# Kernel optimization log

Hardware: AMD Instinct MI355X
Metric: run time of the kernel (lower is better)

Reference implementation:

```python
import jax, jax.numpy as jnp
import numpy as np

EOS_ID = 2
PAD_ID = 0


def setup_inputs() -> dict:
    key = jax.random.key(0)
    ks = jax.random.split(key, 10)
    B, E, H, V, T = 64, 512, 512, 32000, 20
    features = jax.random.normal(ks[0], (B, E), dtype=jnp.float32)
    captions = jax.random.randint(ks[1], (B, T), 0, V)            # unused in policy branch
    lengths = jax.random.randint(ks[2], (B,), 1, T + 1)
    lengths = lengths.at[0].set(T)                                 # make max(lengths) == 20 deterministic
    # parameters (match torch init scales roughly)
    embed_W = jax.random.uniform(ks[3], (V, E), jnp.float32, -0.1, 0.1)
    s = 1.0 / np.sqrt(H)
    W_ih = jax.random.uniform(ks[4], (4 * H, E), jnp.float32, -s, s)
    W_hh = jax.random.uniform(ks[5], (4 * H, H), jnp.float32, -s, s)
    b_ih = jax.random.uniform(ks[6], (4 * H,), jnp.float32, -s, s)
    b_hh = jax.random.uniform(ks[7], (4 * H,), jnp.float32, -s, s)
    linear_W = jax.random.uniform(ks[8], (V, H), jnp.float32, -0.1, 0.1)
    linear_b = jnp.zeros((V,), jnp.float32)
    return {"features": features, "captions": captions, "lengths": lengths,
            "use_policy": 1, "embed_W": embed_W, "W_ih": W_ih, "W_hh": W_hh,
            "b_ih": b_ih, "b_hh": b_hh, "linear_W": linear_W, "linear_b": linear_b}


def _lstm_cell(x, h, c, W_ih, W_hh, b_ih, b_hh):
    # PyTorch gate order: i, f, g, o
    gates = x @ W_ih.T + b_ih + h @ W_hh.T + b_hh        # [B, 4H]
    i, f, g, o = jnp.split(gates, 4, axis=-1)
    i, f, o = jax.nn.sigmoid(i), jax.nn.sigmoid(f), jax.nn.sigmoid(o)
    g = jnp.tanh(g)
    c = f * c + i * g
    h = o * jnp.tanh(c)
    return h, c


def reference(features, captions, lengths, use_policy, embed_W, W_ih, W_hh,
              b_ih, b_hh, linear_W, linear_b):
    # LSTM decode with categorical sampling, stopping per-example at EOS (id 2)
    # and padding remaining steps with id 0 / log_prob 0. The original loops
    # over batch and time with batch-size-1 kernels; here we batch + lax.scan.
    B, H = features.shape[0], W_hh.shape[1]
    T = int(jnp.max(lengths))                            # concrete at trace setup
    step_keys = jax.random.split(jax.random.key(42), T)

    def step(carry, key_t):
        h, c, x, done = carry
        h, c = _lstm_cell(x, h, c, W_ih, W_hh, b_ih, b_hh)
        logits = h @ linear_W.T + linear_b               # [B, V]
        logp = jax.nn.log_softmax(logits, axis=-1)
        tok = jax.random.categorical(key_t, logits)      # [B] int32
        lp = jnp.take_along_axis(logp, tok[:, None], axis=1)[:, 0]
        ids_rec = jnp.where(done, PAD_ID, tok)
        lp_rec = jnp.where(done, 0.0, lp)
        done = done | ((tok == EOS_ID) & ~done)          # EOS token itself is recorded
        x = embed_W[tok]                                 # next-step input embedding
        return (h, c, x, done), (ids_rec, lp_rec)

    init = (jnp.zeros((B, H), features.dtype), jnp.zeros((B, H), features.dtype),
            features, jnp.zeros((B,), bool))
    _, (ids, logps) = jax.lax.scan(step, init, step_keys)
    sampled_ids = jnp.transpose(ids)                     # [B, T]
    saved_log_probs = jnp.transpose(logps)               # [B, T]
    return sampled_ids, saved_log_probs
```

## Files before the change

kernel.cpp:

```cpp
#include <hip/hip_runtime.h>
#include <hip/hip_bf16.h>
#include <stdint.h>
#include <float.h>

#define BB 64
#define EE 512
#define HH 512
#define VV 32000
#define TT 20
#define INV2048 0.00048828125f

typedef _Float16 f16x8 __attribute__((ext_vector_type(8)));
typedef float f32x4 __attribute__((ext_vector_type(4)));

__device__ __host__ __forceinline__ void tf2x32(uint32_t k0, uint32_t k1, uint32_t x0, uint32_t x1,
                                                uint32_t& o0, uint32_t& o1) {
  const uint32_t k2 = k0 ^ k1 ^ 0x1BD11BDAu;
  x0 += k0; x1 += k1;
#define RND(R) { x0 += x1; x1 = (x1 << R) | (x1 >> (32 - R)); x1 ^= x0; }
  RND(13) RND(15) RND(26) RND(6)
  x0 += k1; x1 += k2 + 1u;
  RND(17) RND(29) RND(16) RND(24)
  x0 += k2; x1 += k0 + 2u;
  RND(13) RND(15) RND(26) RND(6)
  x0 += k0; x1 += k1 + 3u;
  RND(17) RND(29) RND(16) RND(24)
  x0 += k1; x1 += k2 + 4u;
  RND(13) RND(15) RND(26) RND(6)
  x0 += k2; x1 += k0 + 5u;
#undef RND
  o0 = x0; o1 = x1;
}

__device__ __forceinline__ float gumbel_for(uint32_t k1t, uint32_t k2t, uint32_t idx) {
  uint32_t o0, o1; tf2x32(k1t, k2t, 0u, idx, o0, o1);
  uint32_t bits = o0 ^ o1;
  uint32_t mant = bits >> 9;
  float f = __uint_as_float(0x3f800000u | mant) - 1.0f;
  float u = mant ? f : 1.1754943508222875e-38f;
  return -logf(-logf(u));
}

struct Part { float bv; int bix; float blog; float m; float s; };

__device__ __forceinline__ void part_combine(Part& P, const Part& Q) {
  if (Q.bv > P.bv || (Q.bv == P.bv && Q.bix < P.bix)) { P.bv = Q.bv; P.bix = Q.bix; P.blog = Q.blog; }
  if (Q.m > P.m) { P.s = P.s * expf(P.m - Q.m) + Q.s; P.m = Q.m; }
  else           { P.s += Q.s * expf(Q.m - P.m); }
}

__global__ __launch_bounds__(256) void k_init(float* __restrict__ hA, float* __restrict__ cT,
                                              int* __restrict__ done) {
  int i = blockIdx.x * 256 + threadIdx.x;
  if (i < HH * BB) { hA[i] = 0.f; cT[i] = 0.f; }
  if (i < BB) done[i] = 0;
}

__global__ __launch_bounds__(256) void k_gates(const float* __restrict__ xin,
                                               const float* __restrict__ hT,
                                               const float* __restrict__ Wih,
                                               const float* __restrict__ Whh,
                                               float* __restrict__ gatesP) {
  const int jt = blockIdx.x;
  const int kc = blockIdx.y;
  const int tx = threadIdx.x;
  __shared__ float a[64][64];
  __shared__ float wj[64][68];
  const int bi = (tx & 15) * 4;
  const int ji = (tx >> 4) * 4;
  float acc[4][4] = {};
  const float* Wsrc = (kc < 4) ? Wih : Whh;
  for (int s = 0; s < 2; ++s) {
    const int kg = kc * 128 + s * 64;
    if (kc < 4) {
      #pragma unroll
      for (int r = 0; r < 4; ++r) {
        int fi = r * 256 + tx;
        int b = fi >> 4, k4 = (fi & 15) * 4;
        const float4 v = *(const float4*)(xin + b * EE + kg + k4);
        a[k4 + 0][b] = v.x; a[k4 + 1][b] = v.y; a[k4 + 2][b] = v.z; a[k4 + 3][b] = v.w;
      }
    } else {
      #pragma unroll
      for (int r = 0; r < 4; ++r) {
        int fi = r * 256 + tx;
        int row = fi >> 4, c4 = (fi & 15) * 4;
        *(float4*)(&a[row][c4]) = *(const float4*)(hT + (kg - 512 + row) * BB + c4);
      }
    }
    const int kcol = kg & 511;
    #pragma unroll
    for (int r = 0; r < 4; ++r) {
      int fi = r * 256 + tx;
      int j = fi >> 4, k4 = (fi & 15) * 4;
      const float4 v = *(const float4*)(Wsrc + (size_t)(jt * 64 + j) * EE + kcol + k4);
      wj[k4 + 0][j] = v.x; wj[k4 + 1][j] = v.y; wj[k4 + 2][j] = v.z; wj[k4 + 3][j] = v.w;
    }
    __syncthreads();
    #pragma unroll 8
    for (int kk = 0; kk < 64; ++kk) {
      const float4 av = *(const float4*)(&a[kk][bi]);
      const float4 wv = *(const float4*)(&wj[kk][ji]);
      const float avx[4] = {av.x, av.y, av.z, av.w};
      const float wvx[4] = {wv.x, wv.y, wv.z, wv.w};
      #pragma unroll
      for (int jj = 0; jj < 4; ++jj)
        #pragma unroll
        for (int bb = 0; bb < 4; ++bb)
          acc[jj][bb] = fmaf(wvx[jj], avx[bb], acc[jj][bb]);
    }
    __syncthreads();
  }
  #pragma unroll
  for (int jj = 0; jj < 4; ++jj) {
    float4 o = make_float4(acc[jj][0], acc[jj][1], acc[jj][2], acc[jj][3]);
    *(float4*)(gatesP + ((size_t)kc * 2048 + jt * 64 + ji + jj) * BB + bi) = o;
  }
}

__global__ __launch_bounds__(256) void k_lstm_update(const float* __restrict__ gatesP,
                                                     const float* __restrict__ b_ih,
                                                     const float* __restrict__ b_hh,
                                                     float* __restrict__ cT,
                                                     float* __restrict__ hT) {
  const int blk = blockIdx.x;
  const int tx = threadIdx.x;
  const int b = tx & 63;
  const int dk = tx >> 6;
  #pragma unroll
  for (int r = 0; r < 2; ++r) {
    const int k = blk * 8 + dk + r * 4;
    float g[4];
    #pragma unroll
    for (int gi = 0; gi < 4; ++gi) {
      const int j = gi * 512 + k;
      float s = 0.f;
      #pragma unroll
      for (int kc = 0; kc < 8; ++kc) s += gatesP[((size_t)kc * 2048 + j) * BB + b];
      g[gi] = s + b_ih[j] + b_hh[j];
    }
    const float ig = 1.f / (1.f + expf(-g[0]));
    const float fg = 1.f / (1.f + expf(-g[1]));
    const float gg = tanhf(g[2]);
    const float og = 1.f / (1.f + expf(-g[3]));
    const float c = fg * cT[k * BB + b] + ig * gg;
    cT[k * BB + b] = c;
    hT[k * BB + b] = og * tanhf(c);
  }
}

__global__ __launch_bounds__(256) void k_lstm_update_frag(const float* __restrict__ gatesP,
                                                          const float* __restrict__ b_ih,
                                                          const float* __restrict__ b_hh,
                                                          float* __restrict__ cT,
                                                          float* __restrict__ hT,
                                                          _Float16* __restrict__ hfh,
                                                          _Float16* __restrict__ hfl) {
  const int blk = blockIdx.x;
  const int tx = threadIdx.x;
  const int b = tx & 63;
  const int dk = tx >> 6;
  #pragma unroll
  for (int r = 0; r < 2; ++r) {
    const int k = blk * 8 + dk + r * 4;
    float g[4];
    #pragma unroll
    for (int gi = 0; gi < 4; ++gi) {
      const int j = gi * 512 + k;
      float s = 0.f;
      #pragma unroll
      for (int kc = 0; kc < 8; ++kc) s += gatesP[((size_t)kc * 2048 + j) * BB + b];
      g[gi] = s + b_ih[j] + b_hh[j];
    }
    const float ig = 1.f / (1.f + expf(-g[0]));
    const float fg = 1.f / (1.f + expf(-g[1]));
    const float gg = tanhf(g[2]);
    const float og = 1.f / (1.f + expf(-g[3]));
    const float c = fg * cT[k * BB + b] + ig * gg;
    cT[k * BB + b] = c;
    const float h = og * tanhf(c);
    hT[k * BB + b] = h;
    const _Float16 hh = (_Float16)h;
    const _Float16 hl = (_Float16)((h - (float)hh) * 2048.0f);
    const int cc = k >> 5, kr = k & 31;
    const int lane = (kr >> 3) * 16 + (b & 15), j = kr & 7, nb = b >> 4;
    const int idx = ((cc * 4 + nb) * 64 + lane) * 8 + j;
    hfh[idx] = hh; hfl[idx] = hl;
  }
}

__global__ __launch_bounds__(256) void k_convW2(const float* __restrict__ LW,
                                                _Float16* __restrict__ Wh,
                                                _Float16* __restrict__ Wl) {
  const int bv = blockIdx.x, bk = blockIdx.y;
  const int tx = threadIdx.x;
  __shared__ float lds[64][65];
  #pragma unroll
  for (int r = 0; r < 4; ++r) {
    const int fi = r * 256 + tx;
    const int vl = fi >> 4, k4 = (fi & 15) * 4;
    const float4 v = *(const float4*)(LW + (size_t)(bv * 64 + vl) * HH + bk * 64 + k4);
    lds[vl][k4] = v.x; lds[vl][k4 + 1] = v.y; lds[vl][k4 + 2] = v.z; lds[vl][k4 + 3] = v.w;
  }
  __syncthreads();
  #pragma unroll
  for (int r = 0; r < 2; ++r) {
    const int u = r * 256 + tx;
    const int frag = u >> 6;
    const int vbl = frag >> 1, cl = frag & 1;
    const int lane = u & 63;
    const int m = lane & 15, lh = lane >> 4;
    f16x8 hi, lo;
    #pragma unroll
    for (int j = 0; j < 8; ++j) {
      const float f = lds[vbl * 16 + m][cl * 32 + lh * 8 + j];
      const _Float16 h = (_Float16)f;
      hi[j] = h;
      lo[j] = (_Float16)((f - (float)h) * 2048.0f);
    }
    const size_t o = (((size_t)(bv * 4 + vbl) * 16 + (bk * 2 + cl)) * 64 + lane) * 8;
    *(f16x8*)(Wh + o) = hi;
    *(f16x8*)(Wl + o) = lo;
  }
}

__global__ __launch_bounds__(256) void k_logits4(const f16x8* __restrict__ Wh,
                                                 const f16x8* __restrict__ Wl,
                                                 const f16x8* __restrict__ hfh,
                                                 const f16x8* __restrict__ hfl,
                                                 const float* __restrict__ lb,
                                                 uint32_t k1t, uint32_t k2t,
                                                 float4* __restrict__ pf4,
                                                 int* __restrict__ pidx) {
  const int wv = threadIdx.x >> 6;
  const int vt = blockIdx.x * 4 + wv;
  const int lane = threadIdx.x & 63;
  __shared__ float red[4][64][5];
  const f32x4 zero = {0.f, 0.f, 0.f, 0.f};
  f32x4 aH[4]  = {zero, zero, zero, zero};
  f32x4 aM1[4] = {zero, zero, zero, zero};
  f32x4 aM2[4] = {zero, zero, zero, zero};
  const size_t wbase = (size_t)vt * 16 * 64 + lane;
  f16x8 whC = Wh[wbase], wlC = Wl[wbase];
  #pragma unroll 4
  for (int c = 0; c < 16; ++c) {
    f16x8 whN, wlN;
    if (c < 15) { whN = Wh[wbase + (c + 1) * 64]; wlN = Wl[wbase + (c + 1) * 64]; }
    #pragma unroll
    for (int nb = 0; nb < 4; ++nb) {
      const f16x8 bh = hfh[(c * 4 + nb) * 64 + lane];
      const f16x8 bl = hfl[(c * 4 + nb) * 64 + lane];
      aH[nb]  = __builtin_amdgcn_mfma_f32_16x16x32_f16(whC, bh, aH[nb], 0, 0, 0);
      aM1[nb] = __builtin_amdgcn_mfma_f32_16x16x32_f16(whC, bl, aM1[nb], 0, 0, 0);
      aM2[nb] = __builtin_amdgcn_mfma_f32_16x16x32_f16(wlC, bh, aM2[nb], 0, 0, 0);
    }
    whC = whN; wlC = wlN;
  }
  const int v0 = vt * 16 + ((lane >> 4) << 2);
  const float4 bias = *(const float4*)(lb + v0);
  const float bb4[4] = {bias.x, bias.y, bias.z, bias.w};
  Part P[4];
  #pragma unroll
  for (int nb = 0; nb < 4; ++nb) {
    const int b = nb * 16 + (lane & 15);
    float lg = aH[nb][0] + (aM1[nb][0] + aM2[nb][0]) * INV2048 + bb4[0];
    Part p;
    p.bv = lg + gumbel_for(k1t, k2t, (uint32_t)(b * VV + v0));
    p.bix = v0; p.blog = lg; p.m = lg; p.s = 1.0f;
    #pragma unroll
    for (int reg = 1; reg < 4; ++reg) {
      float lg2 = aH[nb][reg] + (aM1[nb][reg] + aM2[nb][reg]) * INV2048 + bb4[reg];
      float pe = lg2 + gumbel_for(k1t, k2t, (uint32_t)(b * VV + v0 + reg));
      if (pe > p.bv) { p.bv = pe; p.bix = v0 + reg; p.blog = lg2; }
      if (lg2 > p.m) { p.s = p.s * expf(p.m - lg2) + 1.f; p.m = lg2; }
      else           { p.s += expf(lg2 - p.m); }
    }
    P[nb] = p;
  }
  #pragma unroll
  for (int msk = 16; msk <= 32; msk <<= 1) {
    #pragma unroll
    for (int nb = 0; nb < 4; ++nb) {
      Part Q;
      Q.bv   = __shfl_xor(P[nb].bv, msk, 64);
      Q.bix  = __shfl_xor(P[nb].bix, msk, 64);
      Q.blog = __shfl_xor(P[nb].blog, msk, 64);
      Q.m    = __shfl_xor(P[nb].m, msk, 64);
      Q.s    = __shfl_xor(P[nb].s, msk, 64);
      part_combine(P[nb], Q);
    }
  }
  if (lane < 16) {
    #pragma unroll
    for (int nb = 0; nb < 4; ++nb) {
      const int b = nb * 16 + lane;
      red[wv][b][0] = P[nb].bv; red[wv][b][1] = __int_as_float(P[nb].bix);
      red[wv][b][2] = P[nb].blog; red[wv][b][3] = P[nb].m; red[wv][b][4] = P[nb].s;
    }
  }
  __syncthreads();
  if (threadIdx.x < 64) {
    const int b = threadIdx.x;
    Part Pc;
    Pc.bv = red[0][b][0]; Pc.bix = __float_as_int(red[0][b][1]); Pc.blog = red[0][b][2];
    Pc.m = red[0][b][3]; Pc.s = red[0][b][4];
    #pragma unroll
    for (int w = 1; w < 4; ++w) {
      Part Q;
      Q.bv = red[w][b][0]; Q.bix = __float_as_int(red[w][b][1]); Q.blog = red[w][b][2];
      Q.m = red[w][b][3]; Q.s = red[w][b][4];
      part_combine(Pc, Q);
    }
    pf4[(size_t)blockIdx.x * BB + b] = make_float4(Pc.bv, Pc.blog, Pc.m, Pc.s);
    pidx[blockIdx.x * BB + b] = Pc.bix;
  }
}

__global__ __launch_bounds__(128) void k_logits2(const float* __restrict__ hT,
                                                 const float* __restrict__ LW,
                                                 const float* __restrict__ lb,
                                                 uint32_t k1t, uint32_t k2t,
                                                 float4* __restrict__ pf4,
                                                 int* __restrict__ pidx) {
  const int vt = blockIdx.x;
  const int tx = threadIdx.x;
  __shared__ float lds[5120];
  float* wTs = lds;
  const int vthr = tx & 15;
  const int bthr = tx >> 4;
  const int vi = vthr * 2;
  const int bi = bthr * 8;
  const int vq = tx >> 4;
  const int ks = tx & 15;
  float acc[2][8] = {};
  for (int kt = 0; kt < 8; ++kt) {
    const int kg = kt * 64;
    #pragma unroll
    for (int s = 0; s < 4; ++s) {
      const int kk = ks + 16 * s;
      const size_t rb = (size_t)(vt * 32 + 4 * vq) * HH + kg + kk;
      float w0 = LW[rb];
      float w1 = LW[rb + HH];
      float w2 = LW[rb + 2 * HH];
      float w3 = LW[rb + 3 * HH];
      const int ph = (4 * vq) ^ (4 * (kk & 7));
      *(float4*)&wTs[kk * 32 + ph] = make_float4(w0, w1, w2, w3);
    }
    __syncthreads();
    #pragma unroll 4
    for (int kk = 0; kk < 64; ++kk) {
      const float* hrow = hT + (size_t)(kg + kk) * BB;
      const float4 h0 = *(const float4*)(hrow + bi);
      const float4 h1 = *(const float4*)(hrow + bi + 4);
      const float2 wv = *(const float2*)&wTs[kk * 32 + (vi ^ (4 * (kk & 7)))];
      acc[0][0] = fmaf(wv.x, h0.x, acc[0][0]); acc[0][1] = fmaf(wv.x, h0.y, acc[0][1]);
      acc[0][2] = fmaf(wv.x, h0.z, acc[0][2]); acc[0][3] = fmaf(wv.x, h0.w, acc[0][3]);
      acc[0][4] = fmaf(wv.x, h1.x, acc[0][4]); acc[0][5] = fmaf(wv.x, h1.y, acc[0][5]);
      acc[0][6] = fmaf(wv.x, h1.z, acc[0][6]); acc[0][7] = fmaf(wv.x, h1.w, acc[0][7]);
      acc[1][0] = fmaf(wv.y, h0.x, acc[1][0]); acc[1][1] = fmaf(wv.y, h0.y, acc[1][1]);
      acc[1][2] = fmaf(wv.y, h0.z, acc[1][2]); acc[1][3] = fmaf(wv.y, h0.w, acc[1][3]);
      acc[1][4] = fmaf(wv.y, h1.x, acc[1][4]); acc[1][5] = fmaf(wv.y, h1.y, acc[1][5]);
      acc[1][6] = fmaf(wv.y, h1.z, acc[1][6]); acc[1][7] = fmaf(wv.y, h1.w, acc[1][7]);
    }
    __syncthreads();
  }
  const int v0g = vt * 32 + vi;
  const float bias0 = lb[v0g];
  const float bias1 = lb[v0g + 1];
  float* red = lds;
  #pragma unroll
  for (int bb = 0; bb < 8; ++bb) {
    const int b = bi + bb;
    const float lg0 = acc[0][bb] + bias0;
    const float lg1 = acc[1][bb] + bias1;
    Part p;
    p.bv = lg0 + gumbel_for(k1t, k2t, (uint32_t)(b * VV + v0g));
    p.bix = v0g; p.blog = lg0;
    const float pe1 = lg1 + gumbel_for(k1t, k2t, (uint32_t)(b * VV + v0g + 1));
    if (pe1 > p.bv) { p.bv = pe1; p.bix = v0g + 1; p.blog = lg1; }
    if (lg0 >= lg1) { p.m = lg0; p.s = 1.f + expf(lg1 - lg0); }
    else            { p.m = lg1; p.s = 1.f + expf(lg0 - lg1); }
    const int slot = (b * 16 + vthr) * 5;
    red[slot + 0] = p.bv; red[slot + 1] = __int_as_float(p.bix); red[slot + 2] = p.blog;
    red[slot + 3] = p.m;  red[slot + 4] = p.s;
  }
  __syncthreads();
  if (tx < 64) {
    const int b = tx;
    Part P;
    { const int s0 = (b * 16) * 5;
      P.bv = red[s0]; P.bix = __float_as_int(red[s0 + 1]); P.blog = red[s0 + 2];
      P.m = red[s0 + 3]; P.s = red[s0 + 4]; }
    #pragma unroll
    for (int c = 1; c < 16; ++c) {
      const int s0 = (b * 16 + c) * 5;
      Part Q; Q.bv = red[s0]; Q.bix = __float_as_int(red[s0 + 1]); Q.blog = red[s0 + 2];
      Q.m = red[s0 + 3]; Q.s = red[s0 + 4];
      part_combine(P, Q);
    }
    pf4[(size_t)vt * BB + b] = make_float4(P.bv, P.blog, P.m, P.s);
    pidx[vt * BB + b] = P.bix;
  }
}

__global__ __launch_bounds__(256) void k_sample2(const float4* __restrict__ pf4,
                                                 const int* __restrict__ pidx,
                                                 const float* __restrict__ embW,
                                                 int* __restrict__ done,
                                                 float* __restrict__ x,
                                                 float* __restrict__ out,
                                                 int step, int nvt) {
  const int b = blockIdx.x;
  const int tx = threadIdx.x;
  __shared__ float red[256 * 5];
  __shared__ int stok;
  Part p; p.bv = -FLT_MAX; p.bix = 0x7fffffff; p.blog = 0.f; p.m = -FLT_MAX; p.s = 0.f;
  for (int vt = tx; vt < nvt; vt += 256) {
    float4 q = pf4[(size_t)vt * BB + b];
    Part Q; Q.bv = q.x; Q.blog = q.y; Q.m = q.z; Q.s = q.w; Q.bix = pidx[vt * BB + b];
    part_combine(p, Q);
  }
  red[tx * 5 + 0] = p.bv; red[tx * 5 + 1] = __int_as_float(p.bix); red[tx * 5 + 2] = p.blog;
  red[tx * 5 + 3] = p.m;  red[tx * 5 + 4] = p.s;
  __syncthreads();
  for (int st = 128; st > 0; st >>= 1) {
    if (tx < st) {
      const int s0 = tx * 5, s1 = (tx + st) * 5;
      Part P, Q;
      P.bv = red[s0]; P.bix = __float_as_int(red[s0 + 1]); P.blog = red[s0 + 2]; P.m = red[s0 + 3]; P.s = red[s0 + 4];
      Q.bv = red[s1]; Q.bix = __float_as_int(red[s1 + 1]); Q.blog = red[s1 + 2]; Q.m = red[s1 + 3]; Q.s = red[s1 + 4];
      part_combine(P, Q);
      red[s0] = P.bv; red[s0 + 1] = __int_as_float(P.bix); red[s0 + 2] = P.blog; red[s0 + 3] = P.m; red[s0 + 4] = P.s;
    }
    __syncthreads();
  }
  if (tx == 0) {
    const int tok = __float_as_int(red[1]);
    const float blog = red[2], M = red[3], S = red[4];
    const float lp = blog - (M + logf(S));
    const int dn = done[b];
    out[b * TT + step] = dn ? 0.0f : (float)tok;
    out[BB * TT + b * TT + step] = dn ? 0.0f : lp;
    done[b] = dn | (tok == 2);
    stok = tok;
  }
  __syncthreads();
  const int tok = stok;
  for (int e = tx; e < EE; e += 256) x[b * EE + e] = embW[(size_t)tok * EE + e];
}

extern "C" void kernel_launch(void* const* d_in, const int* in_sizes, int n_in,
                              void* d_out, int out_size, void* d_ws, size_t ws_size,
                              hipStream_t stream) {
  const float* features = (const float*)d_in[0];
  const float* embW     = (const float*)d_in[4];
  const float* Wih      = (const float*)d_in[5];
  const float* Whh      = (const float*)d_in[6];
  const float* bih      = (const float*)d_in[7];
  const float* bhh      = (const float*)d_in[8];
  const float* LW       = (const float*)d_in[9];
  const float* lb       = (const float*)d_in[10];
  float* out = (float*)d_out;

  uint32_t keys[TT][2];
  for (int t = 0; t < TT; ++t) tf2x32(0u, 42u, 0u, (uint32_t)t, keys[t][0], keys[t][1]);

  float* ws = (float*)d_ws;
  float* hA = ws;
  float* hB = ws + 32768;
  float* cT = ws + 65536;
  float* x  = ws + 98304;

  if (ws_size >= (size_t)73000000) {
    float*  gatesP = ws + 131072;
    float4* pf4    = (float4*)(ws + 1179648);
    int*    pidx   = (int*)(ws + 1691648);
    int*    done   = (int*)(ws + 1819648);
    _Float16* hfh  = (_Float16*)(ws + 1819712);
    _Float16* hfl  = (_Float16*)(ws + 1836096);
    _Float16* Whi  = (_Float16*)(ws + 1852480);
    _Float16* Wlo  = (_Float16*)(ws + 10044480);

    k_convW2<<<dim3(500, 8), dim3(256), 0, stream>>>(LW, Whi, Wlo);
    k_init<<<dim3(128), dim3(256), 0, stream>>>(hA, cT, done);
    const float* hin = hA;
    float* hout = hB;
    for (int t = 0; t < TT; ++t) {
      const float* xin = (t == 0) ? features : x;
      k_gates<<<dim3(32, 8), dim3(256), 0, stream>>>(xin, hin, Wih, Whh, gatesP);
      k_lstm_update_frag<<<dim3(64), dim3(256), 0, stream>>>(gatesP, bih, bhh, cT, hout, hfh, hfl);
      k_logits4<<<dim3(500), dim3(256), 0, stream>>>((const f16x8*)Whi, (const f16x8*)Wlo,
                                                     (const f16x8*)hfh, (const f16x8*)hfl,
                                                     lb, keys[t][0], keys[t][1], pf4, pidx);
      k_sample2<<<dim3(64), dim3(256), 0, stream>>>(pf4, pidx, embW, done, x, out, t, 500);
      const float* tmp = hout; hout = (float*)hin; hin = tmp;
    }
  } else {
    float*  gatesP = ws + 131072;
    float4* pf4    = (float4*)(ws + 131072 + 1048576);
    int*    pidx   = (int*)(ws + 131072 + 1048576 + 256000);
    int*    done   = (int*)(ws + 131072 + 1048576 + 256000 + 64000);

    k_init<<<dim3(128), dim3(256), 0, stream>>>(hA, cT, done);
    const float* hin = hA;
    float* hout = hB;
    for (int t = 0; t < TT; ++t) {
      const float* xin = (t == 0) ? features : x;
      k_gates<<<dim3(32, 8), dim3(256), 0, stream>>>(xin, hin, Wih, Whh, gatesP);
      k_lstm_update<<<dim3(64), dim3(256), 0, stream>>>(gatesP, bih, bhh, cT, hout);
      k_logits2<<<dim3(1000), dim3(128), 0, stream>>>(hout, LW, lb, keys[t][0], keys[t][1], pf4, pidx);
      k_sample2<<<dim3(64), dim3(256), 0, stream>>>(pf4, pidx, embW, done, x, out, t, 1000);
      const float* tmp = hout; hout = (float*)hin; hin = tmp;
    }
  }
}
```

Measured before the change: 935.3 us.

## Fuse LSTM gate GEMM and cell update into split-fp16 MFMA kernel

Replaces the FP32 SIMT gates GEMM plus separate reduction/update kernel with one MFMA kernel. It uses split hi/lo fp16 weights, converted once up front, and a concatenated [x;h] operand held in MFMA fragment layout. The sampler now writes the next-step embedding straight into that fragment layout, and the cell kernel writes h into it, which removes the gatesP partial-sum round trip and one launch per step. The risks are the cell kernel's low occupancy (only 32 blocks) and a precision change from the 3-product split-fp16 scheme. The workspace threshold is raised, so this path only runs when the workspace is at least 80 MB.

```diff
diff --git a/kernel.cpp b/kernel.cpp
--- a/kernel.cpp
+++ b/kernel.cpp
@@ -48,6 +48,326 @@
   if (Q.m > P.m) { P.s = P.s * expf(P.m - Q.m) + Q.s; P.m = Q.m; }
   else           { P.s += Q.s * expf(Q.m - P.m); }
 }
+
+
+__global__ __launch_bounds__(256) void k_convW2(const float* __restrict__ LW,
+                                                _Float16* __restrict__ Wh,
+                                                _Float16* __restrict__ Wl) {
+  const int bv = blockIdx.x, bk = blockIdx.y;
+  const int tx = threadIdx.x;
+  __shared__ float lds[64][65];
+  #pragma unroll
+  for (int r = 0; r < 4; ++r) {
+    const int fi = r * 256 + tx;
+    const int vl = fi >> 4, k4 = (fi & 15) * 4;
+    const float4 v = *(const float4*)(LW + (size_t)(bv * 64 + vl) * HH + bk * 64 + k4);
+    lds[vl][k4] = v.x; lds[vl][k4 + 1] = v.y; lds[vl][k4 + 2] = v.z; lds[vl][k4 + 3] = v.w;
+  }
+  __syncthreads();
+  #pragma unroll
+  for (int r = 0; r < 2; ++r) {
+    const int u = r * 256 + tx;
+    const int frag = u >> 6;
+    const int vbl = frag >> 1, cl = frag & 1;
+    const int lane = u & 63;
+    const int m = lane & 15, lh = lane >> 4;
+    f16x8 hi, lo;
+    #pragma unroll
+    for (int j = 0; j < 8; ++j) {
+      const float f = lds[vbl * 16 + m][cl * 32 + lh * 8 + j];
+      const _Float16 h = (_Float16)f;
+      hi[j] = h;
+      lo[j] = (_Float16)((f - (float)h) * 2048.0f);
+    }
+    const size_t o = (((size_t)(bv * 4 + vbl) * 16 + (bk * 2 + cl)) * 64 + lane) * 8;
+    *(f16x8*)(Wh + o) = hi;
+    *(f16x8*)(Wl + o) = lo;
+  }
+}
+
+__global__ __launch_bounds__(256) void k_convG(const float* __restrict__ Wih,
+                                               const float* __restrict__ Whh,
+                                               _Float16* __restrict__ Gh,
+                                               _Float16* __restrict__ Gl) {
+  const int bv = blockIdx.x, bk = blockIdx.y;
+  const int tx = threadIdx.x;
+  __shared__ float lds[64][65];
+  const float* src = (bk < 8) ? Wih : Whh;
+  const int col = (bk < 8) ? bk * 64 : (bk - 8) * 64;
+  #pragma unroll
+  for (int r = 0; r < 4; ++r) {
+    const int fi = r * 256 + tx;
+    const int jl = fi >> 4, k4 = (fi & 15) * 4;
+    const float4 v = *(const float4*)(src + (size_t)(bv * 64 + jl) * 512 + col + k4);
+    lds[jl][k4] = v.x; lds[jl][k4 + 1] = v.y; lds[jl][k4 + 2] = v.z; lds[jl][k4 + 3] = v.w;
+  }
+  __syncthreads();
+  #pragma unroll
+  for (int r = 0; r < 2; ++r) {
+    const int u = r * 256 + tx;
+    const int frag = u >> 6;
+    const int vbl = frag >> 1, cl = frag & 1;
+    const int lane = u & 63;
+    const int m = lane & 15, lh = lane >> 4;
+    f16x8 hi, lo;
+    #pragma unroll
+    for (int j = 0; j < 8; ++j) {
+      const float f = lds[vbl * 16 + m][cl * 32 + lh * 8 + j];
+      const _Float16 h = (_Float16)f;
+      hi[j] = h;
+      lo[j] = (_Float16)((f - (float)h) * 2048.0f);
+    }
+    const size_t o = (((size_t)(bv * 4 + vbl) * 32 + (bk * 2 + cl)) * 64 + lane) * 8;
+    *(f16x8*)(Gh + o) = hi;
+    *(f16x8*)(Gl + o) = lo;
+  }
+}
+
+__global__ __launch_bounds__(256) void k_convX(const float* __restrict__ feat,
+                                               _Float16* __restrict__ xh,
+                                               _Float16* __restrict__ xl) {
+  const int t = blockIdx.x * 256 + threadIdx.x;
+  const int b = t >> 9, e = t & 511;
+  const float f = feat[t];
+  const _Float16 hh = (_Float16)f;
+  const _Float16 hl = (_Float16)((f - (float)hh) * 2048.0f);
+  const int cc = e >> 5, lane2 = ((e & 31) >> 3) * 16 + (b & 15), j2 = e & 7, nb2 = b >> 4;
+  const int fidx = ((cc * 4 + nb2) * 64 + lane2) * 8 + j2;
+  xh[fidx] = hh; xl[fidx] = hl;
+}
+
+__global__ __launch_bounds__(256) void k_init2(float* __restrict__ cT,
+                                               float* __restrict__ xh0f,
+                                               float* __restrict__ xl0f,
+                                               int* __restrict__ done) {
+  const int i = blockIdx.x * 256 + threadIdx.x;
+  cT[i] = 0.f;
+  if (i < 16384) { xh0f[16384 + i] = 0.f; xl0f[16384 + i] = 0.f; }
+  if (i < BB) done[i] = 0;
+}
+
+__global__ __launch_bounds__(256) void k_cell_mfma(const f16x8* __restrict__ Gh,
+                                                   const f16x8* __restrict__ Gl,
+                                                   const f16x8* __restrict__ xbh,
+                                                   const f16x8* __restrict__ xbl,
+                                                   const float* __restrict__ bih,
+                                                   const float* __restrict__ bhh,
+                                                   float* __restrict__ cT,
+                                                   _Float16* __restrict__ hfh,
+                                                   _Float16* __restrict__ hfl,
+                                                   _Float16* __restrict__ nxh,
+                                                   _Float16* __restrict__ nxl) {
+  const int kt = blockIdx.x;
+  const int g = threadIdx.x >> 6;
+  const int lane = threadIdx.x & 63;
+  const int vb = g * 32 + kt;
+  __shared__ float gl[4][16][64];
+  const f32x4 zero = {0.f, 0.f, 0.f, 0.f};
+  f32x4 aH[4]  = {zero, zero, zero, zero};
+  f32x4 aM1[4] = {zero, zero, zero, zero};
+  f32x4 aM2[4] = {zero, zero, zero, zero};
+  const size_t wbase = (size_t)vb * 32 * 64 + lane;
+  f16x8 whC = Gh[wbase], wlC = Gl[wbase];
+  #pragma unroll 4
+  for (int c = 0; c < 32; ++c) {
+    f16x8 whN, wlN;
+    if (c < 31) { whN = Gh[wbase + (c + 1) * 64]; wlN = Gl[wbase + (c + 1) * 64]; }
+    #pragma unroll
+    for (int nb = 0; nb < 4; ++nb) {
+      const f16x8 bh = xbh[(c * 4 + nb) * 64 + lane];
+      const f16x8 bl = xbl[(c * 4 + nb) * 64 + lane];
+      aH[nb]  = __builtin_amdgcn_mfma_f32_16x16x32_f16(whC, bh, aH[nb], 0, 0, 0);
+      aM1[nb] = __builtin_amdgcn_mfma_f32_16x16x32_f16(whC, bl, aM1[nb], 0, 0, 0);
+      aM2[nb] = __builtin_amdgcn_mfma_f32_16x16x32_f16(wlC, bh, aM2[nb], 0, 0, 0);
+    }
+    whC = whN; wlC = wlN;
+  }
+  const int jl0 = (lane >> 4) << 2;
+  const int j0 = g * 512 + kt * 16 + jl0;
+  const float4 bi4 = *(const float4*)(bih + j0);
+  const float4 bh4 = *(const float4*)(bhh + j0);
+  const float bsum[4] = {bi4.x + bh4.x, bi4.y + bh4.y, bi4.z + bh4.z, bi4.w + bh4.w};
+  #pragma unroll
+  for (int nb = 0; nb < 4; ++nb) {
+    const int bcol = nb * 16 + (lane & 15);
+    #pragma unroll
+    for (int reg = 0; reg < 4; ++reg) {
+      gl[g][jl0 + reg][bcol] = aH[nb][reg] + (aM1[nb][reg] + aM2[nb][reg]) * INV2048 + bsum[reg];
+    }
+  }
+  __syncthreads();
+  #pragma unroll
+  for (int r = 0; r < 4; ++r) {
+    const int idx = r * 256 + threadIdx.x;
+    const int kloc = idx >> 6, b = idx & 63;
+    const float gi = gl[0][kloc][b];
+    const float gf = gl[1][kloc][b];
+    const float gg = gl[2][kloc][b];
+    const float go = gl[3][kloc][b];
+    const float ig = 1.f / (1.f + expf(-gi));
+    const float fg = 1.f / (1.f + expf(-gf));
+    const float gv = tanhf(gg);
+    const float og = 1.f / (1.f + expf(-go));
+    const int k = kt * 16 + kloc;
+    const float c = fg * cT[k * BB + b] + ig * gv;
+    cT[k * BB + b] = c;
+    const float h = og * tanhf(c);
+    const _Float16 hh = (_Float16)h;
+    const _Float16 hl = (_Float16)((h - (float)hh) * 2048.0f);
+    const int cc = k >> 5, lane2 = ((k & 31) >> 3) * 16 + (b & 15), j2 = k & 7, nb2 = b >> 4;
+    const int fidx = ((cc * 4 + nb2) * 64 + lane2) * 8 + j2;
+    hfh[fidx] = hh; hfl[fidx] = hl;
+    const int fidx2 = (((16 + cc) * 4 + nb2) * 64 + lane2) * 8 + j2;
+    nxh[fidx2] = hh; nxl[fidx2] = hl;
+  }
+}
+
+__global__ __launch_bounds__(256) void k_logits4(const f16x8* __restrict__ Wh,
+                                                 const f16x8* __restrict__ Wl,
+                                                 const f16x8* __restrict__ hfh,
+                                                 const f16x8* __restrict__ hfl,
+                                                 const float* __restrict__ lb,
+                                                 uint32_t k1t, uint32_t k2t,
+                                                 float4* __restrict__ pf4,
+                                                 int* __restrict__ pidx) {
+  const int wv = threadIdx.x >> 6;
+  const int vt = blockIdx.x * 4 + wv;
+  const int lane = threadIdx.x & 63;
+  __shared__ float red[4][64][5];
+  const f32x4 zero = {0.f, 0.f, 0.f, 0.f};
+  f32x4 aH[4]  = {zero, zero, zero, zero};
+  f32x4 aM1[4] = {zero, zero, zero, zero};
+  f32x4 aM2[4] = {zero, zero, zero, zero};
+  const size_t wbase = (size_t)vt * 16 * 64 + lane;
+  f16x8 whC = Wh[wbase], wlC = Wl[wbase];
+  #pragma unroll 4
+  for (int c = 0; c < 16; ++c) {
+    f16x8 whN, wlN;
+    if (c < 15) { whN = Wh[wbase + (c + 1) * 64]; wlN = Wl[wbase + (c + 1) * 64]; }
+    #pragma unroll
+    for (int nb = 0; nb < 4; ++nb) {
+      const f16x8 bh = hfh[(c * 4 + nb) * 64 + lane];
+      const f16x8 bl = hfl[(c * 4 + nb) * 64 + lane];
+      aH[nb]  = __builtin_amdgcn_mfma_f32_16x16x32_f16(whC, bh, aH[nb], 0, 0, 0);
+      aM1[nb] = __builtin_amdgcn_mfma_f32_16x16x32_f16(whC, bl, aM1[nb], 0, 0, 0);
+      aM2[nb] = __builtin_amdgcn_mfma_f32_16x16x32_f16(wlC, bh, aM2[nb], 0, 0, 0);
+    }
+    whC = whN; wlC = wlN;
+  }
+  const int v0 = vt * 16 + ((lane >> 4) << 2);
+  const float4 bias = *(const float4*)(lb + v0);
+  const float bb4[4] = {bias.x, bias.y, bias.z, bias.w};
+  Part P[4];
+  #pragma unroll
+  for (int nb = 0; nb < 4; ++nb) {
+    const int b = nb * 16 + (lane & 15);
+    float lg = aH[nb][0] + (aM1[nb][0] + aM2[nb][0]) * INV2048 + bb4[0];
+    Part p;
+    p.bv = lg + gumbel_for(k1t, k2t, (uint32_t)(b * VV + v0));
+    p.bix = v0; p.blog = lg; p.m = lg; p.s = 1.0f;
+    #pragma unroll
+    for (int reg = 1; reg < 4; ++reg) {
+      float lg2 = aH[nb][reg] + (aM1[nb][reg] + aM2[nb][reg]) * INV2048 + bb4[reg];
+      float pe = lg2 + gumbel_for(k1t, k2t, (uint32_t)(b * VV + v0 + reg));
+      if (pe > p.bv) { p.bv = pe; p.bix = v0 + reg; p.blog = lg2; }
+      if (lg2 > p.m) { p.s = p.s * expf(p.m - lg2) + 1.f; p.m = lg2; }
+      else           { p.s += expf(lg2 - p.m); }
+    }
+    P[nb] = p;
+  }
+  #pragma unroll
+  for (int msk = 16; msk <= 32; msk <<= 1) {
+    #pragma unroll
+    for (int nb = 0; nb < 4; ++nb) {
+      Part Q;
+      Q.bv   = __shfl_xor(P[nb].bv, msk, 64);
+      Q.bix  = __shfl_xor(P[nb].bix, msk, 64);
+      Q.blog = __shfl_xor(P[nb].blog, msk, 64);
+      Q.m    = __shfl_xor(P[nb].m, msk, 64);
+      Q.s    = __shfl_xor(P[nb].s, msk, 64);
+      part_combine(P[nb], Q);
+    }
+  }
+  if (lane < 16) {
+    #pragma unroll
+    for (int nb = 0; nb < 4; ++nb) {
+      const int b = nb * 16 + lane;
+      red[wv][b][0] = P[nb].bv; red[wv][b][1] = __int_as_float(P[nb].bix);
+      red[wv][b][2] = P[nb].blog; red[wv][b][3] = P[nb].m; red[wv][b][4] = P[nb].s;
+    }
+  }
+  __syncthreads();
+  if (threadIdx.x < 64) {
+    const int b = threadIdx.x;
+    Part Pc;
+    Pc.bv = red[0][b][0]; Pc.bix = __float_as_int(red[0][b][1]); Pc.blog = red[0][b][2];
+    Pc.m = red[0][b][3]; Pc.s = red[0][b][4];
+    #pragma unroll
+    for (int w = 1; w < 4; ++w) {
+      Part Q;
+      Q.bv = red[w][b][0]; Q.bix = __float_as_int(red[w][b][1]); Q.blog = red[w][b][2];
+      Q.m = red[w][b][3]; Q.s = red[w][b][4];
+      part_combine(Pc, Q);
+    }
+    pf4[(size_t)blockIdx.x * BB + b] = make_float4(Pc.bv, Pc.blog, Pc.m, Pc.s);
+    pidx[blockIdx.x * BB + b] = Pc.bix;
+  }
+}
+
+__global__ __launch_bounds__(256) void k_sample3(const float4* __restrict__ pf4,
+                                                 const int* __restrict__ pidx,
+                                                 const float* __restrict__ embW,
+                                                 int* __restrict__ done,
+                                                 _Float16* __restrict__ nxh,
+                                                 _Float16* __restrict__ nxl,
+                                                 float* __restrict__ out,
+                                                 int step) {
+  const int b = blockIdx.x;
+  const int tx = threadIdx.x;
+  __shared__ float red[256 * 5];
+  __shared__ int stok;
+  Part p; p.bv = -FLT_MAX; p.bix = 0x7fffffff; p.blog = 0.f; p.m = -FLT_MAX; p.s = 0.f;
+  for (int vt = tx; vt < 500; vt += 256) {
+    float4 q = pf4[(size_t)vt * BB + b];
+    Part Q; Q.bv = q.x; Q.blog = q.y; Q.m = q.z; Q.s = q.w; Q.bix = pidx[vt * BB + b];
+    part_combine(p, Q);
+  }
+  red[tx * 5 + 0] = p.bv; red[tx * 5 + 1] = __int_as_float(p.bix); red[tx * 5 + 2] = p.blog;
+  red[tx * 5 + 3] = p.m;  red[tx * 5 + 4] = p.s;
+  __syncthreads();
+  for (int st = 128; st > 0; st >>= 1) {
+    if (tx < st) {
+      const int s0 = tx * 5, s1 = (tx + st) * 5;
+      Part P, Q;
+      P.bv = red[s0]; P.bix = __float_as_int(red[s0 + 1]); P.blog = red[s0 + 2]; P.m = red[s0 + 3]; P.s = red[s0 + 4];
+      Q.bv = red[s1]; Q.bix = __float_as_int(red[s1 + 1]); Q.blog = red[s1 + 2]; Q.m = red[s1 + 3]; Q.s = red[s1 + 4];
+      part_combine(P, Q);
+      red[s0] = P.bv; red[s0 + 1] = __int_as_float(P.bix); red[s0 + 2] = P.blog; red[s0 + 3] = P.m; red[s0 + 4] = P.s;
+    }
+    __syncthreads();
+  }
+  if (tx == 0) {
+    const int tok = __float_as_int(red[1]);
+    const float blog = red[2], M = red[3], S = red[4];
+    const float lp = blog - (M + logf(S));
+    const int dn = done[b];
+    out[b * TT + step] = dn ? 0.0f : (float)tok;
+    out[BB * TT + b * TT + step] = dn ? 0.0f : lp;
+    done[b] = dn | (tok == 2);
+    stok = tok;
+  }
+  __syncthreads();
+  const int tok = stok;
+  for (int e = tx; e < EE; e += 256) {
+    const float f = embW[(size_t)tok * EE + e];
+    const _Float16 hh = (_Float16)f;
+    const _Float16 hl = (_Float16)((f - (float)hh) * 2048.0f);
+    const int cc = e >> 5, lane2 = ((e & 31) >> 3) * 16 + (b & 15), j2 = e & 7, nb2 = b >> 4;
+    const int fidx = ((cc * 4 + nb2) * 64 + lane2) * 8 + j2;
+    nxh[fidx] = hh; nxl[fidx] = hl;
+  }
+}
+
 
 __global__ __launch_bounds__(256) void k_init(float* __restrict__ hA, float* __restrict__ cT,
                                               int* __restrict__ done) {
@@ -118,37 +438,6 @@
   }
 }
 
-__global__ __launch_bounds__(256) void k_lstm_update(const float* __restrict__ gatesP,
-                                                     const float* __restrict__ b_ih,
-                                                     const float* __restrict__ b_hh,
-                                                     float* __restrict__ cT,
-                                                     float* __restrict__ hT) {
-  const int blk = blockIdx.x;
-  const int tx = threadIdx.x;
-  const int b = tx & 63;
-  const int dk = tx >> 6;
-  #pragma unroll
-  for (int r = 0; r < 2; ++r) {
-    const int k = blk * 8 + dk + r * 4;
-    float g[4];
-    #pragma unroll
-    for (int gi = 0; gi < 4; ++gi) {
-      const int j = gi * 512 + k;
-      float s = 0.f;
-      #pragma unroll
-      for (int kc = 0; kc < 8; ++kc) s += gatesP[((size_t)kc * 2048 + j) * BB + b];
-      g[gi] = s + b_ih[j] + b_hh[j];
-    }
-    const float ig = 1.f / (1.f + expf(-g[0]));
-    const float fg = 1.f / (1.f + expf(-g[1]));
-    const float gg = tanhf(g[2]);
-    const float og = 1.f / (1.f + expf(-g[3]));
-    const float c = fg * cT[k * BB + b] + ig * gg;
-    cT[k * BB + b] = c;
-    hT[k * BB + b] = og * tanhf(c);
-  }
-}
-
 __global__ __launch_bounds__(256) void k_lstm_update_frag(const float* __restrict__ gatesP,
                                                           const float* __restrict__ b_ih,
                                                           const float* __restrict__ b_hh,
@@ -186,220 +475,6 @@
     const int lane = (kr >> 3) * 16 + (b & 15), j = kr & 7, nb = b >> 4;
     const int idx = ((cc * 4 + nb) * 64 + lane) * 8 + j;
     hfh[idx] = hh; hfl[idx] = hl;
-  }
-}
-
-__global__ __launch_bounds__(256) void k_convW2(const float* __restrict__ LW,
-                                                _Float16* __restrict__ Wh,
-                                                _Float16* __restrict__ Wl) {
-  const int bv = blockIdx.x, bk = blockIdx.y;
-  const int tx = threadIdx.x;
-  __shared__ float lds[64][65];
-  #pragma unroll
-  for (int r = 0; r < 4; ++r) {
-    const int fi = r * 256 + tx;
-    const int vl = fi >> 4, k4 = (fi & 15) * 4;
-    const float4 v = *(const float4*)(LW + (size_t)(bv * 64 + vl) * HH + bk * 64 + k4);
-    lds[vl][k4] = v.x; lds[vl][k4 + 1] = v.y; lds[vl][k4 + 2] = v.z; lds[vl][k4 + 3] = v.w;
-  }
-  __syncthreads();
-  #pragma unroll
-  for (int r = 0; r < 2; ++r) {
-    const int u = r * 256 + tx;
-    const int frag = u >> 6;
-    const int vbl = frag >> 1, cl = frag & 1;
-    const int lane = u & 63;
-    const int m = lane & 15, lh = lane >> 4;
-    f16x8 hi, lo;
-    #pragma unroll
-    for (int j = 0; j < 8; ++j) {
-      const float f = lds[vbl * 16 + m][cl * 32 + lh * 8 + j];
-      const _Float16 h = (_Float16)f;
-      hi[j] = h;
-      lo[j] = (_Float16)((f - (float)h) * 2048.0f);
-    }
-    const size_t o = (((size_t)(bv * 4 + vbl) * 16 + (bk * 2 + cl)) * 64 + lane) * 8;
-    *(f16x8*)(Wh + o) = hi;
-    *(f16x8*)(Wl + o) = lo;
-  }
-}
-
-__global__ __launch_bounds__(256) void k_logits4(const f16x8* __restrict__ Wh,
-                                                 const f16x8* __restrict__ Wl,
-                                                 const f16x8* __restrict__ hfh,
-                                                 const f16x8* __restrict__ hfl,
-                                                 const float* __restrict__ lb,
-                                                 uint32_t k1t, uint32_t k2t,
-                                                 float4* __restrict__ pf4,
-                                                 int* __restrict__ pidx) {
-  const int wv = threadIdx.x >> 6;
-  const int vt = blockIdx.x * 4 + wv;
-  const int lane = threadIdx.x & 63;
-  __shared__ float red[4][64][5];
-  const f32x4 zero = {0.f, 0.f, 0.f, 0.f};
-  f32x4 aH[4]  = {zero, zero, zero, zero};
-  f32x4 aM1[4] = {zero, zero, zero, zero};
-  f32x4 aM2[4] = {zero, zero, zero, zero};
-  const size_t wbase = (size_t)vt * 16 * 64 + lane;
-  f16x8 whC = Wh[wbase], wlC = Wl[wbase];
-  #pragma unroll 4
-  for (int c = 0; c < 16; ++c) {
-    f16x8 whN, wlN;
-    if (c < 15) { whN = Wh[wbase + (c + 1) * 64]; wlN = Wl[wbase + (c + 1) * 64]; }
-    #pragma unroll
-    for (int nb = 0; nb < 4; ++nb) {
-      const f16x8 bh = hfh[(c * 4 + nb) * 64 + lane];
-      const f16x8 bl = hfl[(c * 4 + nb) * 64 + lane];
-      aH[nb]  = __builtin_amdgcn_mfma_f32_16x16x32_f16(whC, bh, aH[nb], 0, 0, 0);
-      aM1[nb] = __builtin_amdgcn_mfma_f32_16x16x32_f16(whC, bl, aM1[nb], 0, 0, 0);
-      aM2[nb] = __builtin_amdgcn_mfma_f32_16x16x32_f16(wlC, bh, aM2[nb], 0, 0, 0);
-    }
-    whC = whN; wlC = wlN;
-  }
-  const int v0 = vt * 16 + ((lane >> 4) << 2);
-  const float4 bias = *(const float4*)(lb + v0);
-  const float bb4[4] = {bias.x, bias.y, bias.z, bias.w};
-  Part P[4];
-  #pragma unroll
-  for (int nb = 0; nb < 4; ++nb) {
-    const int b = nb * 16 + (lane & 15);
-    float lg = aH[nb][0] + (aM1[nb][0] + aM2[nb][0]) * INV2048 + bb4[0];
-    Part p;
-    p.bv = lg + gumbel_for(k1t, k2t, (uint32_t)(b * VV + v0));
-    p.bix = v0; p.blog = lg; p.m = lg; p.s = 1.0f;
-    #pragma unroll
-    for (int reg = 1; reg < 4; ++reg) {
-      float lg2 = aH[nb][reg] + (aM1[nb][reg] + aM2[nb][reg]) * INV2048 + bb4[reg];
-      float pe = lg2 + gumbel_for(k1t, k2t, (uint32_t)(b * VV + v0 + reg));
-      if (pe > p.bv) { p.bv = pe; p.bix = v0 + reg; p.blog = lg2; }
-      if (lg2 > p.m) { p.s = p.s * expf(p.m - lg2) + 1.f; p.m = lg2; }
-      else           { p.s += expf(lg2 - p.m); }
-    }
-    P[nb] = p;
-  }
-  #pragma unroll
-  for (int msk = 16; msk <= 32; msk <<= 1) {
-    #pragma unroll
-    for (int nb = 0; nb < 4; ++nb) {
-      Part Q;
-      Q.bv   = __shfl_xor(P[nb].bv, msk, 64);
-      Q.bix  = __shfl_xor(P[nb].bix, msk, 64);
-      Q.blog = __shfl_xor(P[nb].blog, msk, 64);
-      Q.m    = __shfl_xor(P[nb].m, msk, 64);
-      Q.s    = __shfl_xor(P[nb].s, msk, 64);
-      part_combine(P[nb], Q);
-    }
-  }
-  if (lane < 16) {
-    #pragma unroll
-    for (int nb = 0; nb < 4; ++nb) {
-      const int b = nb * 16 + lane;
-      red[wv][b][0] = P[nb].bv; red[wv][b][1] = __int_as_float(P[nb].bix);
-      red[wv][b][2] = P[nb].blog; red[wv][b][3] = P[nb].m; red[wv][b][4] = P[nb].s;
-    }
-  }
-  __syncthreads();
-  if (threadIdx.x < 64) {
-    const int b = threadIdx.x;
-    Part Pc;
-    Pc.bv = red[0][b][0]; Pc.bix = __float_as_int(red[0][b][1]); Pc.blog = red[0][b][2];
-    Pc.m = red[0][b][3]; Pc.s = red[0][b][4];
-    #pragma unroll
-    for (int w = 1; w < 4; ++w) {
-      Part Q;
-      Q.bv = red[w][b][0]; Q.bix = __float_as_int(red[w][b][1]); Q.blog = red[w][b][2];
-      Q.m = red[w][b][3]; Q.s = red[w][b][4];
-      part_combine(Pc, Q);
-    }
-    pf4[(size_t)blockIdx.x * BB + b] = make_float4(Pc.bv, Pc.blog, Pc.m, Pc.s);
-    pidx[blockIdx.x * BB + b] = Pc.bix;
-  }
-}
-
-__global__ __launch_bounds__(128) void k_logits2(const float* __restrict__ hT,
-                                                 const float* __restrict__ LW,
-                                                 const float* __restrict__ lb,
-                                                 uint32_t k1t, uint32_t k2t,
-                                                 float4* __restrict__ pf4,
-                                                 int* __restrict__ pidx) {
-  const int vt = blockIdx.x;
-  const int tx = threadIdx.x;
-  __shared__ float lds[5120];
-  float* wTs = lds;
-  const int vthr = tx & 15;
-  const int bthr = tx >> 4;
-  const int vi = vthr * 2;
-  const int bi = bthr * 8;
-  const int vq = tx >> 4;
-  const int ks = tx & 15;
-  float acc[2][8] = {};
-  for (int kt = 0; kt < 8; ++kt) {
-    const int kg = kt * 64;
-    #pragma unroll
-    for (int s = 0; s < 4; ++s) {
-      const int kk = ks + 16 * s;
-      const size_t rb = (size_t)(vt * 32 + 4 * vq) * HH + kg + kk;
-      float w0 = LW[rb];
-      float w1 = LW[rb + HH];
-      float w2 = LW[rb + 2 * HH];
-      float w3 = LW[rb + 3 * HH];
-      const int ph = (4 * vq) ^ (4 * (kk & 7));
-      *(float4*)&wTs[kk * 32 + ph] = make_float4(w0, w1, w2, w3);
-    }
-    __syncthreads();
-    #pragma unroll 4
-    for (int kk = 0; kk < 64; ++kk) {
-      const float* hrow = hT + (size_t)(kg + kk) * BB;
-      const float4 h0 = *(const float4*)(hrow + bi);
-      const float4 h1 = *(const float4*)(hrow + bi + 4);
-      const float2 wv = *(const float2*)&wTs[kk * 32 + (vi ^ (4 * (kk & 7)))];
-      acc[0][0] = fmaf(wv.x, h0.x, acc[0][0]); acc[0][1] = fmaf(wv.x, h0.y, acc[0][1]);
-      acc[0][2] = fmaf(wv.x, h0.z, acc[0][2]); acc[0][3] = fmaf(wv.x, h0.w, acc[0][3]);
-      acc[0][4] = fmaf(wv.x, h1.x, acc[0][4]); acc[0][5] = fmaf(wv.x, h1.y, acc[0][5]);
-      acc[0][6] = fmaf(wv.x, h1.z, acc[0][6]); acc[0][7] = fmaf(wv.x, h1.w, acc[0][7]);
-      acc[1][0] = fmaf(wv.y, h0.x, acc[1][0]); acc[1][1] = fmaf(wv.y, h0.y, acc[1][1]);
-      acc[1][2] = fmaf(wv.y, h0.z, acc[1][2]); acc[1][3] = fmaf(wv.y, h0.w, acc[1][3]);
-      acc[1][4] = fmaf(wv.y, h1.x, acc[1][4]); acc[1][5] = fmaf(wv.y, h1.y, acc[1][5]);
-      acc[1][6] = fmaf(wv.y, h1.z, acc[1][6]); acc[1][7] = fmaf(wv.y, h1.w, acc[1][7]);
-    }
-    __syncthreads();
-  }
-  const int v0g = vt * 32 + vi;
-  const float bias0 = lb[v0g];
-  const float bias1 = lb[v0g + 1];
-  float* red = lds;
-  #pragma unroll
-  for (int bb = 0; bb < 8; ++bb) {
-    const int b = bi + bb;
-    const float lg0 = acc[0][bb] + bias0;
-    const float lg1 = acc[1][bb] + bias1;
-    Part p;
-    p.bv = lg0 + gumbel_for(k1t, k2t, (uint32_t)(b * VV + v0g));
-    p.bix = v0g; p.blog = lg0;
-    const float pe1 = lg1 + gumbel_for(k1t, k2t, (uint32_t)(b * VV + v0g + 1));
-    if (pe1 > p.bv) { p.bv = pe1; p.bix = v0g + 1; p.blog = lg1; }
-    if (lg0 >= lg1) { p.m = lg0; p.s = 1.f + expf(lg1 - lg0); }
-    else            { p.m = lg1; p.s = 1.f + expf(lg0 - lg1); }
-    const int slot = (b * 16 + vthr) * 5;
-    red[slot + 0] = p.bv; red[slot + 1] = __int_as_float(p.bix); red[slot + 2] = p.blog;
-    red[slot + 3] = p.m;  red[slot + 4] = p.s;
-  }
-  __syncthreads();
-  if (tx < 64) {
-    const int b = tx;
-    Part P;
-    { const int s0 = (b * 16) * 5;
-      P.bv = red[s0]; P.bix = __float_as_int(red[s0 + 1]); P.blog = red[s0 + 2];
-      P.m = red[s0 + 3]; P.s = red[s0 + 4]; }
-    #pragma unroll
-    for (int c = 1; c < 16; ++c) {
-      const int s0 = (b * 16 + c) * 5;
-      Part Q; Q.bv = red[s0]; Q.bix = __float_as_int(red[s0 + 1]); Q.blog = red[s0 + 2];
-      Q.m = red[s0 + 3]; Q.s = red[s0 + 4];
-      part_combine(P, Q);
-    }
-    pf4[(size_t)vt * BB + b] = make_float4(P.bv, P.blog, P.m, P.s);
-    pidx[vt * BB + b] = P.bix;
   }
 }
 
@@ -466,12 +541,46 @@
   for (int t = 0; t < TT; ++t) tf2x32(0u, 42u, 0u, (uint32_t)t, keys[t][0], keys[t][1]);
 
   float* ws = (float*)d_ws;
-  float* hA = ws;
-  float* hB = ws + 32768;
-  float* cT = ws + 65536;
-  float* x  = ws + 98304;
-
-  if (ws_size >= (size_t)73000000) {
+
+  if (ws_size >= (size_t)80000000) {
+    float*  cT   = ws;
+    int*    done = (int*)(ws + 32768);
+    float4* pf4  = (float4*)(ws + 32832);
+    int*    pidx = (int*)(ws + 160832);
+    _Float16* hfh = (_Float16*)(ws + 192832);
+    _Float16* hfl = (_Float16*)(ws + 209216);
+    float* xb0hf = ws + 225600;
+    float* xb0lf = ws + 258368;
+    float* xb1hf = ws + 291136;
+    float* xb1lf = ws + 323904;
+    _Float16* GhW = (_Float16*)(ws + 356672);
+    _Float16* GlW = (_Float16*)(ws + 1405248);
+    _Float16* Whi = (_Float16*)(ws + 2453824);
+    _Float16* Wlo = (_Float16*)(ws + 10645824);
+
+    _Float16* xbh[2] = {(_Float16*)xb0hf, (_Float16*)xb1hf};
+    _Float16* xbl[2] = {(_Float16*)xb0lf, (_Float16*)xb1lf};
+
+    k_convW2<<<dim3(500, 8), dim3(256), 0, stream>>>(LW, Whi, Wlo);
+    k_convG<<<dim3(32, 16), dim3(256), 0, stream>>>(Wih, Whh, GhW, GlW);
+    k_convX<<<dim3(128), dim3(256), 0, stream>>>(features, xbh[0], xbl[0]);
+    k_init2<<<dim3(128), dim3(256), 0, stream>>>(cT, xb0hf, xb0lf, done);
+
+    for (int t = 0; t < TT; ++t) {
+      const int cur = t & 1, nxt = cur ^ 1;
+      k_cell_mfma<<<dim3(32), dim3(256), 0, stream>>>((const f16x8*)GhW, (const f16x8*)GlW,
+                                                      (const f16x8*)xbh[cur], (const f16x8*)xbl[cur],
+                                                      bih, bhh, cT, hfh, hfl, xbh[nxt], xbl[nxt]);
+      k_logits4<<<dim3(500), dim3(256), 0, stream>>>((const f16x8*)Whi, (const f16x8*)Wlo,
+                                                     (const f16x8*)hfh, (const f16x8*)hfl,
+                                                     lb, keys[t][0], keys[t][1], pf4, pidx);
+      k_sample3<<<dim3(64), dim3(256), 0, stream>>>(pf4, pidx, embW, done, xbh[nxt], xbl[nxt], out, t);
+    }
+  } else {
+    float* hA = ws;
+    float* hB = ws + 32768;
+    float* cT = ws + 65536;
+    float* x  = ws + 98304;
     float*  gatesP = ws + 131072;
     float4* pf4    = (float4*)(ws + 1179648);
     int*    pidx   = (int*)(ws + 1691648);
@@ -495,22 +604,5 @@
       k_sample2<<<dim3(64), dim3(256), 0, stream>>>(pf4, pidx, embW, done, x, out, t, 500);
       const float* tmp = hout; hout = (float*)hin; hin = tmp;
     }
-  } else {
-    float*  gatesP = ws + 131072;
-    float4* pf4    = (float4*)(ws + 131072 + 1048576);
-    int*    pidx   = (int*)(ws + 131072 + 1048576 + 256000);
-    int*    done   = (int*)(ws + 131072 + 1048576 + 256000 + 64000);
-
-    k_init<<<dim3(128), dim3(256), 0, stream>>>(hA, cT, done);
-    const float* hin = hA;
-    float* hout = hB;
-    for (int t = 0; t < TT; ++t) {
-      const float* xin = (t == 0) ? features : x;
-      k_gates<<<dim3(32, 8), dim3(256), 0, stream>>>(xin, hin, Wih, Whh, gatesP);
-      k_lstm_update<<<dim3(64), dim3(256), 0, stream>>>(gatesP, bih, bhh, cT, hout);
-      k_logits2<<<dim3(1000), dim3(128), 0, stream>>>(hout, LW, lb, keys[t][0], keys[t][1], pf4, pidx);
-      k_sample2<<<dim3(64), dim3(256), 0, stream>>>(pf4, pidx, embW, done, x, out, t, 1000);
-      const float* tmp = hout; hout = (float*)hin; hin = tmp;
-    }
-  }
-}
+  }
+}
```

Measured after the change: 1.224 ms. 1.31x slower.
